# Performance work log

Hardware: AMD Instinct MI355X
Metric: run time of the kernel (lower is better)

## Reference

```python
import jax, jax.numpy as jnp
import numpy as np

N_BINS = 15
DELTA = 1.0 / N_BINS


def setup_inputs() -> dict:
    key = jax.random.key(0)
    k1, k2 = jax.random.split(key)
    N, C = 4_000_000, 10
    # scale 5 -> confident softmax -> low collision entropy so bins [0,1) are populated
    logits = jax.random.normal(k1, (N, C), dtype=jnp.float32) * 5.0
    labels = jax.random.randint(k2, (N,), 0, C)
    return {"logits": logits, "labels": labels}


def reference(logits, labels):
    # probs: [N, C]
    probs = jax.nn.softmax(logits, axis=-1)
    # collision entropy H2 per sample: [N]
    u = -jnp.log2(jnp.sum(probs * probs, axis=-1) + 1e-12)
    err_real = (jnp.argmax(probs, axis=-1) != labels).astype(jnp.float32)  # [N]

    n = u.shape[0]
    # bin b covers [b*DELTA, (b+1)*DELTA); samples with u outside [0,1) go to overflow bin
    bin_idx = jnp.floor(u / DELTA).astype(jnp.int32)
    valid = (u >= 0.0) & (u < 1.0)
    seg = jnp.where(valid, bin_idx, N_BINS)

    vf = valid.astype(jnp.float32)
    counts = jax.ops.segment_sum(vf, seg, num_segments=N_BINS + 1)[:N_BINS]
    sum_u = jax.ops.segment_sum(jnp.where(valid, u, 0.0), seg, num_segments=N_BINS + 1)[:N_BINS]
    sum_err = jax.ops.segment_sum(jnp.where(valid, err_real, 0.0), seg, num_segments=N_BINS + 1)[:N_BINS]

    pi = counts / n                      # population weight per bin
    nonempty = counts > 0
    cnt = jnp.where(nonempty, counts, 1.0)
    u_b = sum_u / cnt                    # mean H2 in bin
    err_b = sum_err / cnt                # empirical error rate in bin

    # risk-from-H2 reference curve
    inner = jnp.clip(2.0 * jnp.exp2(-u_b) - 1.0, 0.0, None)
    r_ref = 0.5 * (1.0 - jnp.sqrt(inner))

    gaps = jnp.where(nonempty, jnp.abs(err_b - r_ref) * pi, 0.0)
    return jnp.sum(gaps)
```

## Files before the change

### kernel.cpp

```cpp
#include <hip/hip_runtime.h>
#include <math.h>
#include <stdint.h>

#define NB 15
#define NCOPY 8
#define ACCSTRIDE 64


__global__ __launch_bounds__(256) void bin_kernel(
    const float* __restrict__ logits,
    const int* __restrict__ labels,
    float* __restrict__ acc, int N)
{
    __shared__ float s_acc[3 * NB];
    const int t = threadIdx.x;
    if (t < 3 * NB) s_acc[t] = 0.0f;
    __syncthreads();

    const int lane = t & 63;

    int   pk[NB];
    float su[NB];
#pragma unroll
    for (int b = 0; b < NB; ++b) { pk[b] = 0; su[b] = 0.0f; }

    const long long stride = (long long)gridDim.x * 256;

    for (long long r = (long long)blockIdx.x * 256 + t; r < N; r += stride) {
        const float2* p = (const float2*)(logits + r * 10);
        float lv[10];
#pragma unroll
        for (int j = 0; j < 5; ++j) { float2 w = p[j]; lv[2*j] = w.x; lv[2*j+1] = w.y; }
        const int lab = labels[r];

        float lvl = lv[0];
#pragma unroll
        for (int j = 1; j < 10; ++j) lvl = (lab == j) ? lv[j] : lvl;

        float m = lv[0];
#pragma unroll
        for (int j = 1; j < 10; ++j) m = fmaxf(m, lv[j]);

        const float c = 1.44269504088896340736f;
        float mc = m * c;
        float Z = 0.0f, S = 0.0f;
#pragma unroll
        for (int j = 0; j < 10; ++j) {
            float e = exp2f(fmaf(lv[j], c, -mc));
            Z += e;
            S = fmaf(e, e, S);
        }
        float ratio = S * __builtin_amdgcn_rcpf(Z * Z);
        float u = -log2f(ratio + 1e-12f);

        bool valid = (u >= 0.0f) && (u < 1.0f);
        int bin = -1;
        if (valid) {
            bin = (int)(u * 15.0f);
            if (bin > 14) bin = 14;
        }
        if (!valid) u = 0.0f;
        int e10 = (lvl != m) ? 1 : 0;
        int inc = 1 + (e10 << 16);

#pragma unroll
        for (int b = 0; b < NB; ++b) {
            bool mb = (bin == b);
            pk[b] += mb ? inc : 0;
            su[b] += mb ? u : 0.0f;
        }
    }

#pragma unroll
    for (int b = 0; b < NB; ++b) {
        int   p = pk[b];
        float s = su[b];
#pragma unroll
        for (int off = 1; off < 64; off <<= 1) {
            p += __shfl_xor(p, off, 64);
            s += __shfl_xor(s, off, 64);
        }
        if (lane == 0) {
            atomicAdd(&s_acc[b],          (float)(p & 0xFFFF));
            atomicAdd(&s_acc[NB + b],     s);
            atomicAdd(&s_acc[2 * NB + b], (float)(p >> 16));
        }
    }
    __syncthreads();
    if (t < 3 * NB) {
        float v = s_acc[t];
        if (v != 0.0f)
            atomicAdd(&acc[(blockIdx.x & (NCOPY - 1)) * ACCSTRIDE + t], v);
    }
}

__global__ void finalize_kernel(const float* __restrict__ acc,
                                float* __restrict__ out, float n)
{
    int b = threadIdx.x;
    float gap = 0.0f;
    if (b < NB) {
        float cnt = 0.0f, sumu = 0.0f, serr = 0.0f;
#pragma unroll
        for (int c = 0; c < NCOPY; ++c) {
            cnt  += acc[c * ACCSTRIDE + b];
            sumu += acc[c * ACCSTRIDE + NB + b];
            serr += acc[c * ACCSTRIDE + 2 * NB + b];
        }
        if (cnt > 0.0f) {
            float u_b   = sumu / cnt;
            float err_b = serr / cnt;
            float inner = 2.0f * exp2f(-u_b) - 1.0f;
            if (inner < 0.0f) inner = 0.0f;
            float r_ref = 0.5f * (1.0f - sqrtf(inner));
            gap = fabsf(err_b - r_ref) * (cnt / n);
        }
    }
#pragma unroll
    for (int off = 32; off >= 1; off >>= 1)
        gap += __shfl_xor(gap, off, 64);
    if (b == 0) out[0] = gap;
}

extern "C" void kernel_launch(void* const* d_in, const int* in_sizes, int n_in,
                              void* d_out, int out_size, void* d_ws, size_t ws_size,
                              hipStream_t stream)
{
    const float* logits = (const float*)d_in[0];
    const int*   labels = (const int*)d_in[1];
    const int N = in_sizes[1];

    float* acc = (float*)d_ws;
    hipMemsetAsync(acc, 0, NCOPY * ACCSTRIDE * sizeof(float), stream);

    int blocks = (N + 255) / 256;
    if (blocks > 1024) blocks = 1024;
    if (blocks < 1) blocks = 1;
    bin_kernel<<<blocks, 256, 0, stream>>>(logits, labels, acc, N);
    finalize_kernel<<<1, 64, 0, stream>>>(acc, (float*)d_out, (float)N);
}
```

Measured before the change: 242.8 us.

## Process row pairs with float4 loads and fuse finalize via last-block pattern

Each thread now handles two adjacent rows, loading 80 contiguous bytes as five float4 vectors plus an int2 label load, where it previously used float2 loads for one row. The separate finalize kernel launch is removed: a done counter in the workspace lets the last block to finish read the accumulators through atomics and compute the final gap. This targets load instruction count, memory efficiency and launch overhead, at the cost of higher register pressure from two rows in flight and an extra fence and atomic per block.

```diff
diff --git a/kernel.cpp b/kernel.cpp
--- a/kernel.cpp
+++ b/kernel.cpp
@@ -5,16 +5,54 @@
 #define NB 15
 #define NCOPY 8
 #define ACCSTRIDE 64
+#define DONE_OFF (NCOPY * ACCSTRIDE)
 
+
+__device__ __forceinline__ void row_stats(const float lv[10], int lab, bool rowOK,
+                                          int& bin, float& u, int& inc)
+{
+    float lvl = lv[0];
+#pragma unroll
+    for (int j = 1; j < 10; ++j) lvl = (lab == j) ? lv[j] : lvl;
+
+    float m = lv[0];
+#pragma unroll
+    for (int j = 1; j < 10; ++j) m = fmaxf(m, lv[j]);
+
+    const float c = 1.44269504088896340736f;
+    float mc = m * c;
+    float Z = 0.0f, S = 0.0f;
+#pragma unroll
+    for (int j = 0; j < 10; ++j) {
+        float e = exp2f(fmaf(lv[j], c, -mc));
+        Z += e;
+        S = fmaf(e, e, S);
+    }
+    float ratio = S * __builtin_amdgcn_rcpf(Z * Z);
+    u = -log2f(ratio + 1e-12f);
+
+    bool valid = rowOK && (u >= 0.0f) && (u < 1.0f);
+    bin = -1;
+    if (valid) {
+        bin = (int)(u * 15.0f);
+        if (bin > 14) bin = 14;
+    }
+    if (!valid) u = 0.0f;
+    int e10 = (lvl != m) ? 1 : 0;
+    inc = 1 + (e10 << 16);
+}
 
 __global__ __launch_bounds__(256) void bin_kernel(
     const float* __restrict__ logits,
     const int* __restrict__ labels,
-    float* __restrict__ acc, int N)
+    float* __restrict__ acc,
+    float* __restrict__ out, int N)
 {
     __shared__ float s_acc[3 * NB];
+    __shared__ int s_last;
     const int t = threadIdx.x;
     if (t < 3 * NB) s_acc[t] = 0.0f;
+    if (t == 0) s_last = 0;
     __syncthreads();
 
     const int lane = t & 63;
@@ -24,50 +62,48 @@
 #pragma unroll
     for (int b = 0; b < NB; ++b) { pk[b] = 0; su[b] = 0.0f; }
 
+    const long long nPairs = ((long long)N + 1) >> 1;
     const long long stride = (long long)gridDim.x * 256;
 
-    for (long long r = (long long)blockIdx.x * 256 + t; r < N; r += stride) {
-        const float2* p = (const float2*)(logits + r * 10);
-        float lv[10];
+    for (long long pidx = (long long)blockIdx.x * 256 + t; pidx < nPairs; pidx += stride) {
+        const long long r0 = pidx << 1;
+        const long long r1 = r0 + 1;
+
+        float a[10], b2[10];
+        int labA = 0, labB = 0;
+        bool okB = (r1 < N);
+
+        if (okB) {
+            const float4* p = (const float4*)(logits + r0 * 10);
+            float4 w0 = p[0], w1 = p[1], w2 = p[2], w3 = p[3], w4 = p[4];
+            a[0]=w0.x; a[1]=w0.y; a[2]=w0.z; a[3]=w0.w;
+            a[4]=w1.x; a[5]=w1.y; a[6]=w1.z; a[7]=w1.w;
+            a[8]=w2.x; a[9]=w2.y;
+            b2[0]=w2.z; b2[1]=w2.w;
+            b2[2]=w3.x; b2[3]=w3.y; b2[4]=w3.z; b2[5]=w3.w;
+            b2[6]=w4.x; b2[7]=w4.y; b2[8]=w4.z; b2[9]=w4.w;
+            int2 lb = *(const int2*)(labels + r0);
+            labA = lb.x; labB = lb.y;
+        } else {
+            const float2* p = (const float2*)(logits + r0 * 10);
 #pragma unroll
-        for (int j = 0; j < 5; ++j) { float2 w = p[j]; lv[2*j] = w.x; lv[2*j+1] = w.y; }
-        const int lab = labels[r];
+            for (int j = 0; j < 5; ++j) { float2 w = p[j]; a[2*j] = w.x; a[2*j+1] = w.y; }
+#pragma unroll
+            for (int j = 0; j < 10; ++j) b2[j] = 0.0f;
+            labA = labels[r0];
+        }
 
-        float lvl = lv[0];
-#pragma unroll
-        for (int j = 1; j < 10; ++j) lvl = (lab == j) ? lv[j] : lvl;
-
-        float m = lv[0];
-#pragma unroll
-        for (int j = 1; j < 10; ++j) m = fmaxf(m, lv[j]);
-
-        const float c = 1.44269504088896340736f;
-        float mc = m * c;
-        float Z = 0.0f, S = 0.0f;
-#pragma unroll
-        for (int j = 0; j < 10; ++j) {
-            float e = exp2f(fmaf(lv[j], c, -mc));
-            Z += e;
-            S = fmaf(e, e, S);
-        }
-        float ratio = S * __builtin_amdgcn_rcpf(Z * Z);
-        float u = -log2f(ratio + 1e-12f);
-
-        bool valid = (u >= 0.0f) && (u < 1.0f);
-        int bin = -1;
-        if (valid) {
-            bin = (int)(u * 15.0f);
-            if (bin > 14) bin = 14;
-        }
-        if (!valid) u = 0.0f;
-        int e10 = (lvl != m) ? 1 : 0;
-        int inc = 1 + (e10 << 16);
+        int binA, incA, binB, incB;
+        float uA, uB;
+        row_stats(a,  labA, true, binA, uA, incA);
+        row_stats(b2, labB, okB,  binB, uB, incB);
 
 #pragma unroll
         for (int b = 0; b < NB; ++b) {
-            bool mb = (bin == b);
-            pk[b] += mb ? inc : 0;
-            su[b] += mb ? u : 0.0f;
+            bool mA = (binA == b);
+            bool mB = (binB == b);
+            pk[b] += (mA ? incA : 0) + (mB ? incB : 0);
+            su[b] += (mA ? uA : 0.0f) + (mB ? uB : 0.0f);
         }
     }
 
@@ -92,34 +128,40 @@
         if (v != 0.0f)
             atomicAdd(&acc[(blockIdx.x & (NCOPY - 1)) * ACCSTRIDE + t], v);
     }
-}
 
-__global__ void finalize_kernel(const float* __restrict__ acc,
-                                float* __restrict__ out, float n)
-{
-    int b = threadIdx.x;
-    float gap = 0.0f;
-    if (b < NB) {
-        float cnt = 0.0f, sumu = 0.0f, serr = 0.0f;
+    __threadfence();
+    __syncthreads();
+    if (t == 0) {
+        int old = atomicAdd((int*)(acc + DONE_OFF), 1);
+        if (old == (int)gridDim.x - 1) s_last = 1;
+    }
+    __syncthreads();
+    if (s_last && t < 64) {
+        __threadfence();
+        int b = t;
+        float gap = 0.0f;
+        if (b < NB) {
+            float cnt = 0.0f, sumu = 0.0f, serr = 0.0f;
 #pragma unroll
-        for (int c = 0; c < NCOPY; ++c) {
-            cnt  += acc[c * ACCSTRIDE + b];
-            sumu += acc[c * ACCSTRIDE + NB + b];
-            serr += acc[c * ACCSTRIDE + 2 * NB + b];
+            for (int c = 0; c < NCOPY; ++c) {
+                cnt  += atomicAdd(&acc[c * ACCSTRIDE + b],          0.0f);
+                sumu += atomicAdd(&acc[c * ACCSTRIDE + NB + b],     0.0f);
+                serr += atomicAdd(&acc[c * ACCSTRIDE + 2 * NB + b], 0.0f);
+            }
+            if (cnt > 0.0f) {
+                float u_b   = sumu / cnt;
+                float err_b = serr / cnt;
+                float inner = 2.0f * exp2f(-u_b) - 1.0f;
+                if (inner < 0.0f) inner = 0.0f;
+                float r_ref = 0.5f * (1.0f - sqrtf(inner));
+                gap = fabsf(err_b - r_ref) * (cnt / (float)N);
+            }
         }
-        if (cnt > 0.0f) {
-            float u_b   = sumu / cnt;
-            float err_b = serr / cnt;
-            float inner = 2.0f * exp2f(-u_b) - 1.0f;
-            if (inner < 0.0f) inner = 0.0f;
-            float r_ref = 0.5f * (1.0f - sqrtf(inner));
-            gap = fabsf(err_b - r_ref) * (cnt / n);
-        }
+#pragma unroll
+        for (int off = 32; off >= 1; off >>= 1)
+            gap += __shfl_xor(gap, off, 64);
+        if (b == 0) out[0] = gap;
     }
-#pragma unroll
-    for (int off = 32; off >= 1; off >>= 1)
-        gap += __shfl_xor(gap, off, 64);
-    if (b == 0) out[0] = gap;
 }
 
 extern "C" void kernel_launch(void* const* d_in, const int* in_sizes, int n_in,
@@ -131,11 +173,11 @@
     const int N = in_sizes[1];
 
     float* acc = (float*)d_ws;
-    hipMemsetAsync(acc, 0, NCOPY * ACCSTRIDE * sizeof(float), stream);
+    hipMemsetAsync(acc, 0, (NCOPY * ACCSTRIDE + 16) * sizeof(float), stream);
 
-    int blocks = (N + 255) / 256;
+    const long long nPairs = ((long long)N + 1) >> 1;
+    int blocks = (int)((nPairs + 255) / 256);
     if (blocks > 1024) blocks = 1024;
     if (blocks < 1) blocks = 1;
-    bin_kernel<<<blocks, 256, 0, stream>>>(logits, labels, acc, N);
-    finalize_kernel<<<1, 64, 0, stream>>>(acc, (float*)d_out, (float)N);
+    bin_kernel<<<blocks, 256, 0, stream>>>(logits, labels, acc, (float*)d_out, N);
 }
```

New measurement: 384.5 us. +58.4%, slower.

## Replace per-thread register histograms with per-sample shared-memory atomics

Applied to the files above, without the earlier changes.

Drops the 15-bin per-thread register histograms and their end-of-loop wave shuffle reductions. Each valid sample now does two LDS float atomicAdds, one for the sum of u and one that packs the count and error flag into a single float (1 or 4098). The block later decodes the packed float into count and error before the global atomics. The grid cap is raised to 2048 blocks and a min-blocks launch bound is added to raise occupancy. The packing is exact only while each block's per-bin count stays below 4097 and the packed total stays within float integer precision. LDS atomics that hit the same bin within a wave may serialize.

```diff
diff --git a/kernel.cpp b/kernel.cpp
--- a/kernel.cpp
+++ b/kernel.cpp
@@ -7,22 +7,15 @@
 #define ACCSTRIDE 64
 
 
-__global__ __launch_bounds__(256) void bin_kernel(
+__global__ __launch_bounds__(256, 8) void bin_kernel(
     const float* __restrict__ logits,
     const int* __restrict__ labels,
     float* __restrict__ acc, int N)
 {
-    __shared__ float s_acc[3 * NB];
+    __shared__ float s_acc[2 * NB];
     const int t = threadIdx.x;
-    if (t < 3 * NB) s_acc[t] = 0.0f;
+    if (t < 2 * NB) s_acc[t] = 0.0f;
     __syncthreads();
-
-    const int lane = t & 63;
-
-    int   pk[NB];
-    float su[NB];
-#pragma unroll
-    for (int b = 0; b < NB; ++b) { pk[b] = 0; su[b] = 0.0f; }
 
     const long long stride = (long long)gridDim.x * 256;
 
@@ -53,44 +46,25 @@
         float ratio = S * __builtin_amdgcn_rcpf(Z * Z);
         float u = -log2f(ratio + 1e-12f);
 
-        bool valid = (u >= 0.0f) && (u < 1.0f);
-        int bin = -1;
-        if (valid) {
-            bin = (int)(u * 15.0f);
+        if (u >= 0.0f && u < 1.0f) {
+            int bin = (int)(u * 15.0f);
             if (bin > 14) bin = 14;
-        }
-        if (!valid) u = 0.0f;
-        int e10 = (lvl != m) ? 1 : 0;
-        int inc = 1 + (e10 << 16);
-
-#pragma unroll
-        for (int b = 0; b < NB; ++b) {
-            bool mb = (bin == b);
-            pk[b] += mb ? inc : 0;
-            su[b] += mb ? u : 0.0f;
+            float ce = (lvl != m) ? 4098.0f : 1.0f;
+            atomicAdd(&s_acc[bin], ce);
+            atomicAdd(&s_acc[NB + bin], u);
         }
     }
 
-#pragma unroll
-    for (int b = 0; b < NB; ++b) {
-        int   p = pk[b];
-        float s = su[b];
-#pragma unroll
-        for (int off = 1; off < 64; off <<= 1) {
-            p += __shfl_xor(p, off, 64);
-            s += __shfl_xor(s, off, 64);
-        }
-        if (lane == 0) {
-            atomicAdd(&s_acc[b],          (float)(p & 0xFFFF));
-            atomicAdd(&s_acc[NB + b],     s);
-            atomicAdd(&s_acc[2 * NB + b], (float)(p >> 16));
-        }
-    }
     __syncthreads();
-    if (t < 3 * NB) {
-        float v = s_acc[t];
-        if (v != 0.0f)
-            atomicAdd(&acc[(blockIdx.x & (NCOPY - 1)) * ACCSTRIDE + t], v);
+    if (t < NB) {
+        int v = (int)s_acc[t];
+        int err = v / 4097;
+        int cnt = v - err * 4097 + err;
+        float* base = acc + (blockIdx.x & (NCOPY - 1)) * ACCSTRIDE;
+        if (cnt) atomicAdd(base + t, (float)cnt);
+        if (err) atomicAdd(base + 2 * NB + t, (float)err);
+        float su = s_acc[NB + t];
+        if (su != 0.0f) atomicAdd(base + NB + t, su);
     }
 }
 
@@ -134,7 +108,7 @@
     hipMemsetAsync(acc, 0, NCOPY * ACCSTRIDE * sizeof(float), stream);
 
     int blocks = (N + 255) / 256;
-    if (blocks > 1024) blocks = 1024;
+    if (blocks > 2048) blocks = 2048;
     if (blocks < 1) blocks = 1;
     bin_kernel<<<blocks, 256, 0, stream>>>(logits, labels, acc, N);
     finalize_kernel<<<1, 64, 0, stream>>>(acc, (float*)d_out, (float)N);
```

Result: no change. 241.9 us (-0.3%).
